# Optimization experiments

Measured on AMD Instinct MI355X. Metric: run time of the kernel, lower is better.

## Reference

```python
import jax, jax.numpy as jnp
import numpy as np

VOCAB = 32000
HID = 1024
CUTOFFS = [0, 10000, 20000, 32000]
N_CLUSTERS = 2
DIV = 4
PROJ_DIMS = [HID // DIV**i for i in range(N_CLUSTERS + 1)]  # [1024, 256, 64]
# Faithful to source quirk: n_vocabs = cutoffs[i] + cutoffs[i+1]
LOGIT_DIMS = [CUTOFFS[i] + CUTOFFS[i + 1] for i in range(N_CLUSTERS + 1)]  # [10000, 30000, 52000]


def setup_inputs() -> dict:
    key = jax.random.key(0)
    ks = jax.random.split(key, 16)
    N = 2048
    inp = {
        "x": jax.random.normal(ks[0], (N, HID), dtype=jnp.float32),
        "y": jax.random.randint(ks[1], (N,), 0, VOCAB, dtype=jnp.int64),
    }
    s = 0.02
    # projections: Linear(hidden, proj_dims[i], bias=False); stored as [in, out]
    inp["Wp0"] = jax.random.normal(ks[2], (HID, PROJ_DIMS[0]), dtype=jnp.float32) * s
    inp["Wp1"] = jax.random.normal(ks[3], (HID, PROJ_DIMS[1]), dtype=jnp.float32) * s
    inp["Wp2"] = jax.random.normal(ks[4], (HID, PROJ_DIMS[2]), dtype=jnp.float32) * s
    # logits: Linear(proj_dims[i], LOGIT_DIMS[i]) with bias
    inp["Wl0"] = jax.random.normal(ks[5], (PROJ_DIMS[0], LOGIT_DIMS[0]), dtype=jnp.float32) * s
    inp["bl0"] = jnp.zeros((LOGIT_DIMS[0],), dtype=jnp.float32)
    inp["Wl1"] = jax.random.normal(ks[6], (PROJ_DIMS[1], LOGIT_DIMS[1]), dtype=jnp.float32) * s
    inp["bl1"] = jnp.zeros((LOGIT_DIMS[1],), dtype=jnp.float32)
    inp["Wl2"] = jax.random.normal(ks[7], (PROJ_DIMS[2], LOGIT_DIMS[2]), dtype=jnp.float32) * s
    inp["bl2"] = jnp.zeros((LOGIT_DIMS[2],), dtype=jnp.float32)
    # cluster_logit: Linear(hidden, n_clusters)
    inp["Wc"] = jax.random.normal(ks[8], (HID, N_CLUSTERS), dtype=jnp.float32) * s
    inp["bc"] = jnp.zeros((N_CLUSTERS,), dtype=jnp.float32)
    return inp


def reference(x, y, Wp0, Wp1, Wp2, Wl0, bl0, Wl1, bl1, Wl2, bl2, Wc, bc):
    # head: project (dim-preserving here) then head-vocab logits + cluster logits
    head_proj = x @ Wp0                                   # [N, 1024]
    head_logit = jnp.concatenate(
        [head_proj @ Wl0 + bl0, head_proj @ Wc + bc], axis=1
    )                                                     # [N, 10000 + 2]
    head_lp = jax.nn.log_softmax(head_logit, axis=1)

    nll = jnp.zeros(y.shape, dtype=x.dtype)

    # cluster 0: targets in [0, cutoffs[1])
    m0 = (y >= CUTOFFS[0]) & (y < CUTOFFS[1])
    t0 = jnp.clip(y - CUTOFFS[0], 0, head_lp.shape[1] - 1)
    lp0 = jnp.take_along_axis(head_lp, t0[:, None], axis=1)[:, 0]
    nll = jnp.where(m0, -lp0, nll)

    # tail clusters: small projection GEMM + log_softmax + gather, combined via masks
    tails = [(Wp1, Wl1, bl1), (Wp2, Wl2, bl2)]
    for i, (Wp, Wl, bl) in enumerate(tails, start=1):
        l, r = CUTOFFS[i], CUTOFFS[i + 1]
        mask = (y >= l) & (y < r)
        t = jnp.clip(y - l, 0, Wl.shape[1] - 1)
        tail_lp = jax.nn.log_softmax((x @ Wp) @ Wl + bl, axis=1)  # [N, LOGIT_DIMS[i]]
        # faithful to source: head column -i (reversed cluster order quirk)
        lp = head_lp[:, -i] + jnp.take_along_axis(tail_lp, t[:, None], axis=1)[:, 0]
        nll = jnp.where(mask, -lp, nll)

    return nll
```

## Files before the change

kernel.cpp:

```cpp
#include <hip/hip_runtime.h>
#include <math.h>

#define HID 1024
#define NROWS 2048

typedef __attribute__((ext_vector_type(8))) short short8;
typedef __attribute__((ext_vector_type(4))) short short4_t;
typedef __attribute__((ext_vector_type(4))) float f32x4;

__device__ __forceinline__ short f2bf(float f) {
  union { float f; unsigned u; } v; v.f = f;
  unsigned r = v.u + 0x7fffu + ((v.u >> 16) & 1u);
  return (short)(r >> 16);
}
__device__ __forceinline__ float bf2f(short s) {
  union { unsigned u; float f; } v; v.u = ((unsigned)(unsigned short)s) << 16;
  return v.f;
}
__device__ __forceinline__ float wave_sum(float a) {
#pragma unroll
  for (int off = 32; off; off >>= 1) a += __shfl_xor(a, off, 64);
  return a;
}

__device__ __forceinline__ void transpose_tile(const float* __restrict__ W,
                                               short* __restrict__ BT,
                                               int K, int N, int Npad, int tn,
                                               int b, int tid) {
  __shared__ float T[32][33];
  const int n0 = (b % tn) * 32, k0 = (b / tn) * 32;
  const int r = tid >> 3, c = (tid & 7) * 4;
  float v0 = 0.f, v1 = 0.f, v2 = 0.f, v3 = 0.f;
  const float* p = &W[(size_t)(k0 + r) * N];
  if (n0 + c + 3 < N) {
    v0 = p[n0 + c]; v1 = p[n0 + c + 1]; v2 = p[n0 + c + 2]; v3 = p[n0 + c + 3];
  } else {
    if (n0 + c + 0 < N) v0 = p[n0 + c + 0];
    if (n0 + c + 1 < N) v1 = p[n0 + c + 1];
    if (n0 + c + 2 < N) v2 = p[n0 + c + 2];
  }
  T[r][c] = v0; T[r][c + 1] = v1; T[r][c + 2] = v2; T[r][c + 3] = v3;
  __syncthreads();
  const int nl = tid >> 3, kl = (tid & 7) * 4;
  const int n = n0 + nl;
  if (n < Npad) {
    short4_t o;
    o.x = (n < N) ? f2bf(T[kl + 0][nl]) : (short)0;
    o.y = (n < N) ? f2bf(T[kl + 1][nl]) : (short)0;
    o.z = (n < N) ? f2bf(T[kl + 2][nl]) : (short)0;
    o.w = (n < N) ? f2bf(T[kl + 3][nl]) : (short)0;
    *(short4_t*)&BT[(size_t)n * K + k0 + kl] = o;
  }
}

__global__ __launch_bounds__(256) void prep1(
    const float* __restrict__ x, const int* __restrict__ y,
    const float* __restrict__ Wp0, const float* __restrict__ Wp1,
    const float* __restrict__ Wp2,
    short* __restrict__ xb,
    int* __restrict__ counts, int* __restrict__ slot_of_row,
    int* __restrict__ rows1, int* __restrict__ rows2,
    short* __restrict__ T0, short* __restrict__ T1, short* __restrict__ T2) {
  const int tid = threadIdx.x;
  int b = blockIdx.x;
  if (b == 0) {
    __shared__ int c1s, c2s;
    if (tid == 0) { c1s = 0; c2s = 0; }
    __syncthreads();
    for (int r = tid; r < NROWS; r += 256) {
      const int yy = y[r];
      if (yy >= 20000) {
        const int s = atomicAdd(&c2s, 1);
        slot_of_row[r] = s; rows2[s] = r;
      } else if (yy >= 10000) {
        const int s = atomicAdd(&c1s, 1);
        slot_of_row[r] = s; rows1[s] = r;
      } else {
        slot_of_row[r] = -1;
      }
    }
    __syncthreads();
    if (tid == 0) { counts[0] = NROWS; counts[1] = c1s; counts[2] = c2s; }
    return;
  }
  if (b <= 2048) {
    const int i = ((b - 1) * 256 + tid) * 4;
    short4_t o;
    o.x = f2bf(x[i + 0]); o.y = f2bf(x[i + 1]);
    o.z = f2bf(x[i + 2]); o.w = f2bf(x[i + 3]);
    *(short4_t*)&xb[i] = o;
    return;
  }
  b -= 2049;
  if (b < 1024)               transpose_tile(Wp0, T0, 1024, 1024, 1024, 32, b, tid);
  else if ((b -= 1024) < 256) transpose_tile(Wp1, T1, 1024, 256, 256, 8, b, tid);
  else { b -= 256;            transpose_tile(Wp2, T2, 1024, 64, 128, 4, b, tid); }
}

__device__ __forceinline__ void mfma_mainloop(const short* aB[4], const short* bB[4],
                                              short* As, short* Bs,
                                              f32x4 acc[4][4],
                                              int K, int w, int lane) {
  const int quad = lane >> 4, ln = lane & 15;
  const int wm = w >> 1, wn = w & 1;
  const int l7 = ln & 7;
  for (int kt = 0; kt < K; kt += 64) {
#pragma unroll
    for (int i = 0; i < 4; ++i) {
      const int row = w * 32 + i * 8;
      __builtin_amdgcn_global_load_lds(
          (const __attribute__((address_space(1))) void*)(aB[i] + kt),
          (__attribute__((address_space(3))) void*)(As + row * 64), 16, 0, 0);
      __builtin_amdgcn_global_load_lds(
          (const __attribute__((address_space(1))) void*)(bB[i] + kt),
          (__attribute__((address_space(3))) void*)(Bs + row * 64), 16, 0, 0);
    }
    __syncthreads();
#pragma unroll
    for (int ks = 0; ks < 2; ++ks) {
      const int kcs = ks * 4 + quad;
      short8 af[4], bfr[4];
#pragma unroll
      for (int mt = 0; mt < 4; ++mt) {
        const int row = wm * 64 + mt * 16 + ln;
        af[mt] = *(const short8*)(As + ((row * 8 + (kcs ^ l7)) << 3));
      }
#pragma unroll
      for (int nt = 0; nt < 4; ++nt) {
        const int rowb = wn * 64 + nt * 16 + ln;
        bfr[nt] = *(const short8*)(Bs + ((rowb * 8 + (kcs ^ l7)) << 3));
      }
#pragma unroll
      for (int mt = 0; mt < 4; ++mt)
#pragma unroll
        for (int nt = 0; nt < 4; ++nt)
          acc[mt][nt] = __builtin_amdgcn_mfma_f32_16x16x32_bf16(
              af[mt], bfr[nt], acc[mt][nt], 0, 0, 0);
    }
    __syncthreads();
  }
}


__global__ __launch_bounds__(256) void launch2(
    const short* __restrict__ xb,
    const short* __restrict__ WpT0, const short* __restrict__ WpT1,
    const short* __restrict__ WpT2,
    short* __restrict__ P0b, short* __restrict__ P1c, short* __restrict__ P2c,
    const int* __restrict__ rows1, const int* __restrict__ rows2,
    const int* __restrict__ counts,
    const float* __restrict__ Wl0, const float* __restrict__ Wl1,
    const float* __restrict__ Wl2,
    short* __restrict__ WlT0, short* __restrict__ WlT1,
    short* __restrict__ WlT2) {
  int b = blockIdx.x;
  const int tid = threadIdx.x;
  if (b >= 176) {
    b -= 176;
    if (b < 10112)               transpose_tile(Wl0, WlT0, 1024, 10000, 10112, 316, b, tid);
    else if ((b -= 10112) < 7520) transpose_tile(Wl1, WlT1, 256, 30000, 30080, 940, b, tid);
    else { b -= 7520;             transpose_tile(Wl2, WlT2, 64, 52000, 52096, 1628, b, tid); }
    return;
  }
  const short* BT; short* C; int N, r0, c0, cnt;
  const int* rowlist = nullptr;
  if (b < 128) {
    BT = WpT0; C = P0b; N = 1024;
    c0 = (b & 7) * 128; r0 = (b >> 3) * 128; cnt = NROWS;
  } else if (b < 160) {
    b -= 128; BT = WpT1; C = P1c; N = 256;
    c0 = (b & 1) * 128; r0 = (b >> 1) * 128; rowlist = rows1; cnt = counts[1];
  } else {
    b -= 160; BT = WpT2; C = P2c; N = 64;
    c0 = 0; r0 = b * 128; rowlist = rows2; cnt = counts[2];
  }
  if (r0 >= cnt) return;

  __shared__ short As[128 * 64];
  __shared__ short Bs[128 * 64];
  const int w = tid >> 6, lane = tid & 63;
  const int quad = lane >> 4, ln = lane & 15;
  const int wm = w >> 1, wn = w & 1;
  const int rsub = lane >> 3;
  const int kc = (lane & 7) ^ rsub;
  const int K = 1024;

  const short* aB[4]; const short* bB[4];
#pragma unroll
  for (int i = 0; i < 4; ++i) {
    const int sl = r0 + w * 32 + i * 8 + rsub;
    const int ar = rowlist ? rowlist[sl < cnt ? sl : cnt - 1] : sl;
    aB[i] = xb + (size_t)ar * K + kc * 8;
    bB[i] = BT + (size_t)(c0 + w * 32 + i * 8 + rsub) * K + kc * 8;
  }

  f32x4 acc[4][4];
  const f32x4 zero = {0.f, 0.f, 0.f, 0.f};
#pragma unroll
  for (int i = 0; i < 4; ++i)
#pragma unroll
    for (int j = 0; j < 4; ++j) acc[i][j] = zero;
  mfma_mainloop(aB, bB, As, Bs, acc, K, w, lane);
#pragma unroll
  for (int mt = 0; mt < 4; ++mt)
#pragma unroll
    for (int r = 0; r < 4; ++r) {
      const int grow = r0 + wm * 64 + mt * 16 + quad * 4 + r;
#pragma unroll
      for (int nt = 0; nt < 4; ++nt) {
        const int cg = c0 + wn * 64 + nt * 16 + ln;
        if (cg < N) C[(size_t)grow * N + cg] = f2bf(acc[mt][nt][r]);
      }
    }
}

template <int K, int NCOLS, int NSPLIT, bool CS_SLOW>
__device__ __forceinline__ void logit_phase(
    const short* __restrict__ A, const short* __restrict__ BT,
    const float* __restrict__ bias, float* __restrict__ ps,
    short* As, short* Bs,
    int nrb, int csbase, int ncs, int lid, int tid) {
  float* psL = (float*)As;
  const int w = tid >> 6, lane = tid & 63;
  const int quad = lane >> 4, ln = lane & 15;
  const int wm = w >> 1, wn = w & 1;
  const int rsub = lane >> 3;
  const int kc = (lane & 7) ^ rsub;
  const int l7 = ln & 15 & 7;
  const int T = nrb * ncs;
  for (int t = lid; t < T; t += 128) {
    const int rb = CS_SLOW ? (t % nrb) : (t / ncs);
    const int cs = csbase + (CS_SLOW ? (t / nrb) : (t % ncs));
    const int r0 = rb * 128, c0 = cs * 128;

    const short* aB[4]; const short* bB[4];
#pragma unroll
    for (int i = 0; i < 4; ++i) {
      aB[i] = A + (size_t)(r0 + w * 32 + i * 8 + rsub) * K + kc * 8;
      bB[i] = BT + (size_t)(c0 + w * 32 + i * 8 + rsub) * K + kc * 8;
    }
    f32x4 acc[4][4];
    const f32x4 zero = {0.f, 0.f, 0.f, 0.f};
#pragma unroll
    for (int i = 0; i < 4; ++i)
#pragma unroll
      for (int j = 0; j < 4; ++j) acc[i][j] = zero;

    __syncthreads();
    for (int kt = 0; kt < K; kt += 64) {
#pragma unroll
      for (int i = 0; i < 4; ++i) {
        const int row = w * 32 + i * 8;
        __builtin_amdgcn_global_load_lds(
            (const __attribute__((address_space(1))) void*)(aB[i] + kt),
            (__attribute__((address_space(3))) void*)(As + row * 64), 16, 0, 0);
        __builtin_amdgcn_global_load_lds(
            (const __attribute__((address_space(1))) void*)(bB[i] + kt),
            (__attribute__((address_space(3))) void*)(Bs + row * 64), 16, 0, 0);
      }
      __syncthreads();
#pragma unroll
      for (int ks = 0; ks < 2; ++ks) {
        const int kcs = ks * 4 + quad;
        short8 af[4], bfr[4];
#pragma unroll
        for (int mt = 0; mt < 4; ++mt) {
          const int row = wm * 64 + mt * 16 + ln;
          af[mt] = *(const short8*)(As + ((row * 8 + (kcs ^ l7)) << 3));
        }
#pragma unroll
        for (int nt = 0; nt < 4; ++nt) {
          const int rowb = wn * 64 + nt * 16 + ln;
          bfr[nt] = *(const short8*)(Bs + ((rowb * 8 + (kcs ^ l7)) << 3));
        }
#pragma unroll
        for (int mt = 0; mt < 4; ++mt)
#pragma unroll
          for (int nt = 0; nt < 4; ++nt)
            acc[mt][nt] = __builtin_amdgcn_mfma_f32_16x16x32_bf16(
                af[mt], bfr[nt], acc[mt][nt], 0, 0, 0);
      }
      __syncthreads();
    }

    float bv[4];
#pragma unroll
    for (int nt = 0; nt < 4; ++nt) {
      const int cg = c0 + wn * 64 + nt * 16 + ln;
      bv[nt] = (cg < NCOLS) ? bias[cg] : -1.0e30f;
    }
#pragma unroll
    for (int mt = 0; mt < 4; ++mt)
#pragma unroll
      for (int r = 0; r < 4; ++r) {
        float s = 0.f;
#pragma unroll
        for (int nt = 0; nt < 4; ++nt)
          s += __expf(acc[mt][nt][r] + bv[nt]);
#pragma unroll
        for (int off = 1; off < 16; off <<= 1) s += __shfl_xor(s, off, 64);
        if (ln == 0) psL[wn * 128 + wm * 64 + mt * 16 + quad * 4 + r] = s;
      }
    __syncthreads();
    if (tid < 128)
      ps[(size_t)(r0 + tid) * NSPLIT + cs] = psL[tid] + psL[128 + tid];
  }
}

__global__ __launch_bounds__(256) void logit_persist(
    const short* __restrict__ P0b, const short* __restrict__ WlT0,
    const float* __restrict__ bl0, float* __restrict__ psh,
    const short* __restrict__ P1c, const short* __restrict__ WlT1,
    const float* __restrict__ bl1, float* __restrict__ ps1,
    const short* __restrict__ P2c, const short* __restrict__ WlT2,
    const float* __restrict__ bl2, float* __restrict__ ps2,
    const int* __restrict__ counts) {
  __shared__ short As[128 * 64];
  __shared__ short Bs[128 * 64];
  const int tid = threadIdx.x;
  const int xcd = blockIdx.x & 7;
  const int lid = blockIdx.x >> 3;
  const int nrb1 = (counts[1] + 127) >> 7;
  const int nrb2 = (counts[2] + 127) >> 7;

  logit_phase<1024, 10000, 79, false>(P0b, WlT0, bl0, psh, As, Bs,
                                      16, xcd * 10, (xcd < 7) ? 10 : 9, lid, tid);
  logit_phase<256, 30000, 235, true>(P1c, WlT1, bl1, ps1, As, Bs,
                                     nrb1, xcd * 30, (xcd < 7) ? 30 : 25, lid, tid);
  logit_phase<64, 52000, 407, true>(P2c, WlT2, bl2, ps2, As, Bs,
                                    nrb2, xcd * 51, (xcd < 7) ? 51 : 50, lid, tid);
}

__global__ __launch_bounds__(256) void finalize(
    const short* __restrict__ P0b, const short* __restrict__ P1c,
    const short* __restrict__ P2c,
    const short* __restrict__ WlT0, const float* __restrict__ bl0,
    const short* __restrict__ WlT1, const float* __restrict__ bl1,
    const short* __restrict__ WlT2, const float* __restrict__ bl2,
    const float* __restrict__ Wc, const float* __restrict__ bc,
    const int* __restrict__ y, const int* __restrict__ slot_of_row,
    const float* __restrict__ psh, const float* __restrict__ ps1,
    const float* __restrict__ ps2, float* __restrict__ out) {
  const int lane = threadIdx.x & 63;
  const int row = blockIdx.x * 4 + (threadIdx.x >> 6);

  float a0 = 0.f, a1 = 0.f;
  for (int k = lane; k < HID; k += 64) {
    const float p = bf2f(P0b[(size_t)row * HID + k]);
    a0 += p * Wc[2 * k];
    a1 += p * Wc[2 * k + 1];
  }
  a0 = wave_sum(a0);
  a1 = wave_sum(a1);
  const float cl0 = a0 + bc[0], cl1 = a1 + bc[1];

  float S = 0.f;
  for (int i = lane; i < 79; i += 64) S += psh[(size_t)row * 79 + i];
  S = wave_sum(S) + __expf(cl0) + __expf(cl1);
  const float lse = logf(S);

  const int yy = y[row];
  float nll;
  if (yy < 10000) {
    const short* pr = P0b + (size_t)row * 1024;
    const short* wr = WlT0 + (size_t)yy * 1024;
    float a = 0.f;
    for (int kk = lane * 4; kk < 1024; kk += 256) {
      const short4_t p = *(const short4_t*)(pr + kk);
      const short4_t wv = *(const short4_t*)(wr + kk);
      a += bf2f(p.x) * bf2f(wv.x) + bf2f(p.y) * bf2f(wv.y)
         + bf2f(p.z) * bf2f(wv.z) + bf2f(p.w) * bf2f(wv.w);
    }
    a = wave_sum(a);
    nll = -((a + bl0[yy]) - lse);
  } else if (yy < 20000) {
    const int t = yy - 10000;
    const int slot = slot_of_row[row];
    float S1 = 0.f;
    for (int i = lane; i < 235; i += 64) S1 += ps1[(size_t)slot * 235 + i];
    S1 = wave_sum(S1);
    const short* pr = P1c + (size_t)slot * 256;
    const short* wr = WlT1 + (size_t)t * 256;
    const int kk = lane * 4;
    const short4_t p = *(const short4_t*)(pr + kk);
    const short4_t wv = *(const short4_t*)(wr + kk);
    float a = bf2f(p.x) * bf2f(wv.x) + bf2f(p.y) * bf2f(wv.y)
            + bf2f(p.z) * bf2f(wv.z) + bf2f(p.w) * bf2f(wv.w);
    a = wave_sum(a);
    nll = -((cl1 - lse) + ((a + bl1[t]) - logf(S1)));
  } else {
    const int t = yy - 20000;
    const int slot = slot_of_row[row];
    float S2 = 0.f;
    for (int i = lane; i < 407; i += 64) S2 += ps2[(size_t)slot * 407 + i];
    S2 = wave_sum(S2);
    float a = 0.f;
    if (lane < 16) {
      const short* pr = P2c + (size_t)slot * 64;
      const short* wr = WlT2 + (size_t)t * 64;
      const int kk = lane * 4;
      const short4_t p = *(const short4_t*)(pr + kk);
      const short4_t wv = *(const short4_t*)(wr + kk);
      a = bf2f(p.x) * bf2f(wv.x) + bf2f(p.y) * bf2f(wv.y)
        + bf2f(p.z) * bf2f(wv.z) + bf2f(p.w) * bf2f(wv.w);
    }
    a = wave_sum(a);
    nll = -((cl0 - lse) + ((a + bl2[t]) - logf(S2)));
  }
  if (lane == 0) out[row] = nll;
}

extern "C" void kernel_launch(void* const* d_in, const int* in_sizes, int n_in,
                              void* d_out, int out_size, void* d_ws, size_t ws_size,
                              hipStream_t stream) {
  const float* x   = (const float*)d_in[0];
  const int*   y   = (const int*)d_in[1];
  const float* Wp0 = (const float*)d_in[2];
  const float* Wp1 = (const float*)d_in[3];
  const float* Wp2 = (const float*)d_in[4];
  const float* Wl0 = (const float*)d_in[5];
  const float* bl0 = (const float*)d_in[6];
  const float* Wl1 = (const float*)d_in[7];
  const float* bl1 = (const float*)d_in[8];
  const float* Wl2 = (const float*)d_in[9];
  const float* bl2 = (const float*)d_in[10];
  const float* Wc  = (const float*)d_in[11];
  const float* bc  = (const float*)d_in[12];
  float* out = (float*)d_out;

  float* fws = (float*)d_ws;
  float* psh = fws; fws += (size_t)NROWS * 79;
  float* ps1 = fws; fws += (size_t)NROWS * 235;
  float* ps2 = fws; fws += (size_t)NROWS * 407;
  int* iws = (int*)fws;
  int* counts      = iws; iws += 4;
  int* slot_of_row = iws; iws += NROWS;
  int* rows1       = iws; iws += NROWS;
  int* rows2       = iws; iws += NROWS;
  short* sp = (short*)iws;
  short* xb   = sp; sp += (size_t)NROWS * 1024;
  short* P0b  = sp; sp += (size_t)NROWS * 1024;
  short* P1c  = sp; sp += (size_t)NROWS * 256;
  short* P2c  = sp; sp += (size_t)NROWS * 64;
  short* WpT0 = sp; sp += (size_t)1024 * 1024;
  short* WpT1 = sp; sp += (size_t)256 * 1024;
  short* WpT2 = sp; sp += (size_t)128 * 1024;
  short* WlT0 = sp; sp += (size_t)10112 * 1024;
  short* WlT1 = sp; sp += (size_t)30080 * 256;
  short* WlT2 = sp; sp += (size_t)52096 * 64;

  dim3 blk(256);
  prep1<<<dim3(3457), blk, 0, stream>>>(x, y, Wp0, Wp1, Wp2, xb,
                                        counts, slot_of_row, rows1, rows2,
                                        WpT0, WpT1, WpT2);
  launch2<<<dim3(21064), blk, 0, stream>>>(xb, WpT0, WpT1, WpT2,
                                           P0b, P1c, P2c, rows1, rows2, counts,
                                           Wl0, Wl1, Wl2, WlT0, WlT1, WlT2);
  logit_persist<<<dim3(1024), blk, 0, stream>>>(
      P0b, WlT0, bl0, psh, P1c, WlT1, bl1, ps1, P2c, WlT2, bl2, ps2, counts);
  finalize<<<dim3(NROWS / 4), blk, 0, stream>>>(
      P0b, P1c, P2c, WlT0, bl0, WlT1, bl1, WlT2, bl2, Wc, bc, y, slot_of_row,
      psh, ps1, ps2, out);
}
```

Baseline: 320.1 us.

## Reschedule weight transposes to overlap head logit GEMM with tail transposes

Moves the Wl0 transpose into the first prep kernel and leaves the projection GEMM as a small standalone kernel. A new kernel runs the head-vocab logit GEMM (one tile per block, 1280 blocks) in the same grid as the Wl1/Wl2 transposes, so compute and memory-bound work share the GPU. Tail logits get their own persistent kernel. The aim is to stop the transposes and the tiny projection GEMM from serializing in front of the logit work, at the cost of one extra kernel launch.

```diff
diff --git a/kernel.cpp b/kernel.cpp
--- a/kernel.cpp
+++ b/kernel.cpp
@@ -53,14 +53,15 @@
   }
 }
 
-__global__ __launch_bounds__(256) void prep1(
+__global__ __launch_bounds__(256) void prep(
     const float* __restrict__ x, const int* __restrict__ y,
     const float* __restrict__ Wp0, const float* __restrict__ Wp1,
-    const float* __restrict__ Wp2,
+    const float* __restrict__ Wp2, const float* __restrict__ Wl0,
     short* __restrict__ xb,
     int* __restrict__ counts, int* __restrict__ slot_of_row,
     int* __restrict__ rows1, int* __restrict__ rows2,
-    short* __restrict__ T0, short* __restrict__ T1, short* __restrict__ T2) {
+    short* __restrict__ T0, short* __restrict__ T1, short* __restrict__ T2,
+    short* __restrict__ T3) {
   const int tid = threadIdx.x;
   int b = blockIdx.x;
   if (b == 0) {
@@ -94,7 +95,8 @@
   b -= 2049;
   if (b < 1024)               transpose_tile(Wp0, T0, 1024, 1024, 1024, 32, b, tid);
   else if ((b -= 1024) < 256) transpose_tile(Wp1, T1, 1024, 256, 256, 8, b, tid);
-  else { b -= 256;            transpose_tile(Wp2, T2, 1024, 64, 128, 4, b, tid); }
+  else if ((b -= 256) < 128)  transpose_tile(Wp2, T2, 1024, 64, 128, 4, b, tid);
+  else { b -= 128;            transpose_tile(Wl0, T3, 1024, 10000, 10112, 316, b, tid); }
 }
 
 __device__ __forceinline__ void mfma_mainloop(const short* aB[4], const short* bB[4],
@@ -142,26 +144,15 @@
 }
 
 
-__global__ __launch_bounds__(256) void launch2(
+__global__ __launch_bounds__(256) void proj_all(
     const short* __restrict__ xb,
     const short* __restrict__ WpT0, const short* __restrict__ WpT1,
     const short* __restrict__ WpT2,
     short* __restrict__ P0b, short* __restrict__ P1c, short* __restrict__ P2c,
     const int* __restrict__ rows1, const int* __restrict__ rows2,
-    const int* __restrict__ counts,
-    const float* __restrict__ Wl0, const float* __restrict__ Wl1,
-    const float* __restrict__ Wl2,
-    short* __restrict__ WlT0, short* __restrict__ WlT1,
-    short* __restrict__ WlT2) {
+    const int* __restrict__ counts) {
   int b = blockIdx.x;
   const int tid = threadIdx.x;
-  if (b >= 176) {
-    b -= 176;
-    if (b < 10112)               transpose_tile(Wl0, WlT0, 1024, 10000, 10112, 316, b, tid);
-    else if ((b -= 10112) < 7520) transpose_tile(Wl1, WlT1, 256, 30000, 30080, 940, b, tid);
-    else { b -= 7520;             transpose_tile(Wl2, WlT2, 64, 52000, 52096, 1628, b, tid); }
-    return;
-  }
   const short* BT; short* C; int N, r0, c0, cnt;
   const int* rowlist = nullptr;
   if (b < 128) {
@@ -219,16 +210,16 @@
     const short* __restrict__ A, const short* __restrict__ BT,
     const float* __restrict__ bias, float* __restrict__ ps,
     short* As, short* Bs,
-    int nrb, int csbase, int ncs, int lid, int tid) {
+    int nrb, int csbase, int ncs, int lid, int step, int tid) {
   float* psL = (float*)As;
   const int w = tid >> 6, lane = tid & 63;
   const int quad = lane >> 4, ln = lane & 15;
   const int wm = w >> 1, wn = w & 1;
   const int rsub = lane >> 3;
   const int kc = (lane & 7) ^ rsub;
-  const int l7 = ln & 15 & 7;
+  const int l7 = ln & 7;
   const int T = nrb * ncs;
-  for (int t = lid; t < T; t += 128) {
+  for (int t = lid; t < T; t += step) {
     const int rb = CS_SLOW ? (t % nrb) : (t / ncs);
     const int cs = csbase + (CS_SLOW ? (t / nrb) : (t % ncs));
     const int r0 = rb * 128, c0 = cs * 128;
@@ -307,9 +298,29 @@
   }
 }
 
-__global__ __launch_bounds__(256) void logit_persist(
+__global__ __launch_bounds__(256) void head_mix(
     const short* __restrict__ P0b, const short* __restrict__ WlT0,
     const float* __restrict__ bl0, float* __restrict__ psh,
+    const float* __restrict__ Wl1, const float* __restrict__ Wl2,
+    short* __restrict__ WlT1, short* __restrict__ WlT2) {
+  int b = blockIdx.x;
+  const int tid = threadIdx.x;
+  if (b >= 1280) {
+    b -= 1280;
+    if (b < 7520) transpose_tile(Wl1, WlT1, 256, 30000, 30080, 940, b, tid);
+    else          transpose_tile(Wl2, WlT2, 64, 52000, 52096, 1628, b - 7520, tid);
+    return;
+  }
+  __shared__ short As[128 * 64];
+  __shared__ short Bs[128 * 64];
+  const int xcd = b & 7;
+  const int j = b >> 3;
+  const int nch = (xcd < 7) ? 10 : 9;
+  logit_phase<1024, 10000, 79, false>(P0b, WlT0, bl0, psh, As, Bs,
+                                      16, xcd * 10, nch, j, 100000, tid);
+}
+
+__global__ __launch_bounds__(256) void tail_logit(
     const short* __restrict__ P1c, const short* __restrict__ WlT1,
     const float* __restrict__ bl1, float* __restrict__ ps1,
     const short* __restrict__ P2c, const short* __restrict__ WlT2,
@@ -322,13 +333,12 @@
   const int lid = blockIdx.x >> 3;
   const int nrb1 = (counts[1] + 127) >> 7;
   const int nrb2 = (counts[2] + 127) >> 7;
-
-  logit_phase<1024, 10000, 79, false>(P0b, WlT0, bl0, psh, As, Bs,
-                                      16, xcd * 10, (xcd < 7) ? 10 : 9, lid, tid);
   logit_phase<256, 30000, 235, true>(P1c, WlT1, bl1, ps1, As, Bs,
-                                     nrb1, xcd * 30, (xcd < 7) ? 30 : 25, lid, tid);
+                                     nrb1, xcd * 30, (xcd < 7) ? 30 : 25,
+                                     lid, 128, tid);
   logit_phase<64, 52000, 407, true>(P2c, WlT2, bl2, ps2, As, Bs,
-                                    nrb2, xcd * 51, (xcd < 7) ? 51 : 50, lid, tid);
+                                    nrb2, xcd * 51, (xcd < 7) ? 51 : 50,
+                                    lid, 128, tid);
 }
 
 __global__ __launch_bounds__(256) void finalize(
@@ -450,14 +460,15 @@
   short* WlT2 = sp; sp += (size_t)52096 * 64;
 
   dim3 blk(256);
-  prep1<<<dim3(3457), blk, 0, stream>>>(x, y, Wp0, Wp1, Wp2, xb,
+  prep<<<dim3(13569), blk, 0, stream>>>(x, y, Wp0, Wp1, Wp2, Wl0, xb,
                                         counts, slot_of_row, rows1, rows2,
-                                        WpT0, WpT1, WpT2);
-  launch2<<<dim3(21064), blk, 0, stream>>>(xb, WpT0, WpT1, WpT2,
-                                           P0b, P1c, P2c, rows1, rows2, counts,
-                                           Wl0, Wl1, Wl2, WlT0, WlT1, WlT2);
-  logit_persist<<<dim3(1024), blk, 0, stream>>>(
-      P0b, WlT0, bl0, psh, P1c, WlT1, bl1, ps1, P2c, WlT2, bl2, ps2, counts);
+                                        WpT0, WpT1, WpT2, WlT0);
+  proj_all<<<dim3(176), blk, 0, stream>>>(xb, WpT0, WpT1, WpT2,
+                                          P0b, P1c, P2c, rows1, rows2, counts);
+  head_mix<<<dim3(12056), blk, 0, stream>>>(P0b, WlT0, bl0, psh,
+                                            Wl1, Wl2, WlT1, WlT2);
+  tail_logit<<<dim3(1024), blk, 0, stream>>>(P1c, WlT1, bl1, ps1,
+                                             P2c, WlT2, bl2, ps2, counts);
   finalize<<<dim3(NROWS / 4), blk, 0, stream>>>(
       P0b, P1c, P2c, WlT0, bl0, WlT1, bl1, WlT2, bl2, Wc, bc, y, slot_of_row,
       psh, ps1, ps2, out);
```

Result: no change. 322.8 us (+0.8%).
